# Optimization experiments

Measured on AMD Instinct MI355X. Metric: run time of the kernel, lower is better.

The kernel has to match this reference:

```python
import jax, jax.numpy as jnp
import numpy as np

N, D, E = 65536, 64, 4096


def setup_inputs() -> dict:
    key = jax.random.key(0)
    k1, k2, k3 = jax.random.split(key, 3)
    return {
        "input_data": jax.random.normal(k1, (N, D), dtype=jnp.float32),
        "codebook": jax.random.normal(k2, (E, D), dtype=jnp.float32),
        "dither": jax.random.uniform(k3, (E - 1,), dtype=jnp.float32),
        "entries": E,
    }


def _decode(frac_idx, cb):
    # linear interpolation between consecutive codebook entries
    e = cb.shape[0]
    ii = jnp.clip(jnp.floor(frac_idx), 0, e - 2).astype(jnp.int32)
    r = (frac_idx - ii.astype(frac_idx.dtype))[..., None]
    return (1.0 - r) * cb[ii] + r * cb[ii + 1]


def reference(input_data, codebook, dither, entries):
    cur = codebook[:entries]                                   # (E, D)
    # fractional_index = dither + linspace(0, E-2, E-1) == dither + arange(E-1)
    frac = dither + jnp.arange(entries - 1, dtype=dither.dtype)
    dithered_cb = _decode(frac, cur)                           # (E-1, D)
    # squared euclidean distances via expansion (same argmin as (x-c)^2 sum)
    x2 = jnp.sum(input_data * input_data, axis=1, keepdims=True)   # (N, 1)
    c2 = jnp.sum(dithered_cb * dithered_cb, axis=1)                # (E-1,)
    dist = x2 - 2.0 * (input_data @ dithered_cb.T) + c2[None, :]   # (N, E-1)
    integer_index = jnp.argmin(dist, axis=1)                       # (N,)
    quantized = _decode(integer_index.astype(input_data.dtype), dithered_cb)
    # perplexity = exp(entropy of codebook usage) over `entries` bins
    counts = jnp.zeros((entries,), dtype=jnp.float32).at[integer_index].add(1.0)
    avg_probs = counts / input_data.shape[0]
    perplexity = jnp.exp(-jnp.sum(avg_probs * jnp.log(avg_probs + 1e-10)))
    return quantized, perplexity, integer_index
```

## Files before the change

kernel.cpp:

```cpp
#include <hip/hip_runtime.h>
#include <math.h>


constexpr int D = 64;
constexpr int CHUNK = 128;
constexpr int NTILES = CHUNK / 16;
constexpr int E_PAD = 4096;
constexpr int NCH = E_PAD / CHUNK;
constexpr float TAU = 0.01f;
constexpr int NSLICE = 8;
constexpr int SLICE_E = E_PAD / NSLICE;

typedef __attribute__((ext_vector_type(8))) short bf16x8;
typedef __attribute__((ext_vector_type(4))) float f32x4;

__device__ inline unsigned short f2bf(float x) {
  unsigned int u = __float_as_uint(x);
  u = (u + 0x7fffu + ((u >> 16) & 1u)) >> 16;
  return (unsigned short)u;
}
__device__ inline float bf2f(unsigned short h) {
  return __uint_as_float(((unsigned int)h) << 16);
}

__device__ __forceinline__ void gll16(const void* g, void* l) {
  __builtin_amdgcn_global_load_lds(
      (const __attribute__((address_space(1))) unsigned int*)g,
      (__attribute__((address_space(3))) unsigned int*)l, 16, 0, 0);
}
__device__ __forceinline__ void gll4(const void* g, void* l) {
  __builtin_amdgcn_global_load_lds(
      (const __attribute__((address_space(1))) unsigned int*)g,
      (__attribute__((address_space(3))) unsigned int*)l, 4, 0, 0);
}

__global__ __launch_bounds__(64) void build_kernel(
    const float* __restrict__ cb, const float* __restrict__ dither,
    float* __restrict__ dcb, unsigned short* __restrict__ dcbh,
    unsigned short* __restrict__ dcbl, float* __restrict__ c2h, int E, int Em1) {
  int i = blockIdx.x;
  int k = threadIdx.x;
  if (i >= Em1) {
    dcb[(size_t)i * D + k] = 0.f;
    dcbh[(size_t)i * D + k] = 0;
    dcbl[(size_t)i * D + k] = 0;
    if (k == 0) c2h[i] = 3.0e38f;
    return;
  }
  float frac = dither[i] + (float)i;
  int ii = (int)floorf(frac);
  ii = max(0, min(ii, E - 2));
  float r = frac - (float)ii;
  float v = (1.0f - r) * cb[(size_t)ii * D + k] + r * cb[(size_t)(ii + 1) * D + k];
  dcb[(size_t)i * D + k] = v;
  unsigned short h = f2bf(v);
  unsigned short l = f2bf(v - bf2f(h));
  dcbh[(size_t)i * D + k] = h;
  dcbl[(size_t)i * D + k] = l;
  float s = v * v;
#pragma unroll
  for (int off = 32; off > 0; off >>= 1) s += __shfl_down(s, off, 64);
  if (k == 0) c2h[i] = 0.5f * s;
}

__global__ __launch_bounds__(512) void vq_mfma_kernel(
    const float* __restrict__ X, const unsigned short* __restrict__ dcbh,
    const unsigned short* __restrict__ dcbl, const float* __restrict__ c2h,
    int* __restrict__ out_i1, float* __restrict__ out_gap, int N) {
  __shared__ unsigned short s_h[2][CHUNK * D];
  __shared__ unsigned short s_l[2][CHUNK * D];
  __shared__ float s_c2[2][CHUNK];

  const int tid = threadIdx.x;
  const int lane = tid & 63;
  const int wv = tid >> 6;
  const int col = lane & 15;
  const int kg = lane >> 4;
  const int rowbase = blockIdx.x * 128 + wv * 16;

  const float* xp = X + (size_t)(rowbase + col) * D + kg * 8;
  bf16x8 ah0, ah1, al0, al1;
#pragma unroll
  for (int i = 0; i < 8; ++i) {
    float x0 = xp[i], x1 = xp[32 + i];
    unsigned short h0 = f2bf(x0), h1 = f2bf(x1);
    ah0[i] = (short)h0; ah1[i] = (short)h1;
    al0[i] = (short)f2bf(x0 - bf2f(h0));
    al1[i] = (short)f2bf(x1 - bf2f(h1));
  }

  float b1[4], b2[4];
  int i1[4];
#pragma unroll
  for (int r = 0; r < 4; ++r) { b1[r] = -3.4e38f; b2[r] = -3.4e38f; i1[r] = 0; }

  const int xs = col & 7;

  auto stage = [&](int ch, int buf) {
#pragma unroll
    for (int i = 0; i < 2; ++i) {
      const int u = (wv * 2 + i) * 64 + lane;
      const int e = u >> 3, g = u & 7;
      const size_t goff = (((size_t)(ch * CHUNK + e)) << 6) + ((g ^ (e & 7)) << 3);
      char* dst_h = (char*)s_h[buf] + (size_t)(wv * 2 + i) * 1024;
      char* dst_l = (char*)s_l[buf] + (size_t)(wv * 2 + i) * 1024;
      gll16(dcbh + goff, dst_h);
      gll16(dcbl + goff, dst_l);
    }
    if (wv < 2) {
      gll4(c2h + ch * CHUNK + wv * 64 + lane, (char*)s_c2[buf] + wv * 256);
    }
  };

  stage(0, 0);
  __syncthreads();
  int cur = 0;

  for (int ch = 0; ch < NCH; ++ch) {
    const int ebase = ch * CHUNK;
    if (ch + 1 < NCH) stage(ch + 1, cur ^ 1);

#pragma unroll
    for (int t = 0; t < NTILES; ++t) {
      const int el = t * 16 + col;
      const char* bb = (const char*)s_h[cur] + el * 128;
      const char* ll = (const char*)s_l[cur] + el * 128;
      bf16x8 bh0 = *(const bf16x8*)(bb + ((kg ^ xs) << 4));
      bf16x8 bh1 = *(const bf16x8*)(bb + (((kg + 4) ^ xs) << 4));
      bf16x8 bl0 = *(const bf16x8*)(ll + ((kg ^ xs) << 4));
      bf16x8 bl1 = *(const bf16x8*)(ll + (((kg + 4) ^ xs) << 4));
      f32x4 acc = {0.f, 0.f, 0.f, 0.f};
      acc = __builtin_amdgcn_mfma_f32_16x16x32_bf16(ah0, bh0, acc, 0, 0, 0);
      acc = __builtin_amdgcn_mfma_f32_16x16x32_bf16(ah1, bh1, acc, 0, 0, 0);
      acc = __builtin_amdgcn_mfma_f32_16x16x32_bf16(ah0, bl0, acc, 0, 0, 0);
      acc = __builtin_amdgcn_mfma_f32_16x16x32_bf16(ah1, bl1, acc, 0, 0, 0);
      acc = __builtin_amdgcn_mfma_f32_16x16x32_bf16(al0, bh0, acc, 0, 0, 0);
      acc = __builtin_amdgcn_mfma_f32_16x16x32_bf16(al1, bh1, acc, 0, 0, 0);
      float hc2 = s_c2[cur][el];
      int colg = ebase + el;
#pragma unroll
      for (int r = 0; r < 4; ++r) {
        float s = acc[r] - hc2;
        bool gt = s > b1[r];
        b2[r] = __builtin_amdgcn_fmed3f(b2[r], s, b1[r]);
        b1[r] = fmaxf(b1[r], s);
        i1[r] = gt ? colg : i1[r];
      }
    }

    __syncthreads();
    cur ^= 1;
  }

#pragma unroll
  for (int m = 1; m < 16; m <<= 1) {
#pragma unroll
    for (int r = 0; r < 4; ++r) {
      float ob1 = __shfl_xor(b1[r], m, 64);
      float ob2 = __shfl_xor(b2[r], m, 64);
      int oi1 = __shfl_xor(i1[r], m, 64);
      float loser = fminf(b1[r], ob1);
      b2[r] = fmaxf(fmaxf(b2[r], ob2), loser);
      bool take = (ob1 > b1[r]) || (ob1 == b1[r] && oi1 < i1[r]);
      b1[r] = take ? ob1 : b1[r];
      i1[r] = take ? oi1 : i1[r];
    }
  }
  if (col == 0) {
#pragma unroll
    for (int r = 0; r < 4; ++r) {
      int row = rowbase + kg * 4 + r;
      out_i1[row] = i1[r];
      out_gap[row] = b1[r] - b2[r];
    }
  }
}

__global__ __launch_bounds__(64) void finish_kernel(
    const int* __restrict__ out_i1, const float* __restrict__ out_gap,
    const float* __restrict__ dcb, float* __restrict__ outq,
    float* __restrict__ outidx, float* __restrict__ counts,
    int* __restrict__ rescue_n, int* __restrict__ rescue_list, int N) {
  const int lane = threadIdx.x;
  const int rowbase = blockIdx.x * 64;
  const int row = rowbase + lane;
  int bi = out_i1[row];
  float gap2 = 2.0f * out_gap[row];
  outidx[row] = (float)bi;
  if (gap2 < TAU) {
    int p = atomicAdd(rescue_n, 1);
    rescue_list[p] = row;
  } else {
    atomicAdd(&counts[bi], 1.0f);
  }
  for (int r = 0; r < 64; ++r) {
    int idx_r = __shfl(bi, r, 64);
    outq[(size_t)(rowbase + r) * D + lane] = dcb[(size_t)idx_r * D + lane];
  }
}

__global__ __launch_bounds__(64) void rescue_scan_kernel(
    const float* __restrict__ X, const float* __restrict__ dcb,
    const float* __restrict__ c2h, const int* __restrict__ rescue_n,
    const int* __restrict__ rescue_list,
    float* __restrict__ pd, int* __restrict__ pi) {
  const int lane = threadIdx.x;
  const int nu = (*rescue_n) * NSLICE;
  for (int u = blockIdx.x; u < nu; u += gridDim.x) {
    const int li = u >> 3;
    const int sl = u & (NSLICE - 1);
    const int row = rescue_list[li];

    const float4* xr = (const float4*)(X + (size_t)row * D);
    float4 x[16];
#pragma unroll
    for (int k = 0; k < 16; ++k) x[k] = xr[k];

    float best = 3.4e38f;
    int bidx = 0x7fffffff;
    const int e0 = sl * SLICE_E;
#pragma unroll 2
    for (int j = 0; j < SLICE_E / 64; ++j) {
      const int e = e0 + j * 64 + lane;
      const float4* cp = (const float4*)(dcb + (size_t)e * D);
      float d0 = 0.f, d1 = 0.f, d2 = 0.f, d3 = 0.f;
#pragma unroll
      for (int k = 0; k < 16; ++k) {
        float4 c = cp[k];
        d0 = fmaf(x[k].x, c.x, d0);
        d1 = fmaf(x[k].y, c.y, d1);
        d2 = fmaf(x[k].z, c.z, d2);
        d3 = fmaf(x[k].w, c.w, d3);
      }
      float d = c2h[e] - ((d0 + d1) + (d2 + d3));
      if (d < best) { best = d; bidx = e; }
    }
#pragma unroll
    for (int m = 1; m < 64; m <<= 1) {
      float od = __shfl_xor(best, m, 64);
      int oi = __shfl_xor(bidx, m, 64);
      if (od < best || (od == best && oi < bidx)) { best = od; bidx = oi; }
    }
    if (lane == 0) { pd[u] = best; pi[u] = bidx; }
  }
}

__global__ __launch_bounds__(64) void rescue_fin_kernel(
    const float* __restrict__ dcb, const int* __restrict__ rescue_n,
    const int* __restrict__ rescue_list, const float* __restrict__ pd,
    const int* __restrict__ pi, float* __restrict__ outq,
    float* __restrict__ outidx, float* __restrict__ counts) {
  const int lane = threadIdx.x;
  const int nr = *rescue_n;
  for (int li = blockIdx.x; li < nr; li += gridDim.x) {
    const int row = rescue_list[li];
    float d = (lane < NSLICE) ? pd[li * NSLICE + lane] : 3.5e38f;
    int ix = (lane < NSLICE) ? pi[li * NSLICE + lane] : 0x7fffffff;
#pragma unroll
    for (int m = 1; m < NSLICE; m <<= 1) {
      float od = __shfl_xor(d, m, 64);
      int oi = __shfl_xor(ix, m, 64);
      if (od < d || (od == d && oi < ix)) { d = od; ix = oi; }
    }
    int bfin = __shfl(ix, 0, 64);
    if (lane == 0) {
      outidx[row] = (float)bfin;
      atomicAdd(&counts[bfin], 1.0f);
    }
    outq[(size_t)row * D + lane] = dcb[(size_t)bfin * D + lane];
  }
}

__global__ __launch_bounds__(256) void vq_perp_kernel(
    const float* __restrict__ counts, float* __restrict__ out, int E, float invN) {
  __shared__ float red[4];
  float s = 0.f;
  for (int j = threadIdx.x; j < E; j += 256) {
    float p = counts[j] * invN;
    s += p * logf(p + 1e-10f);
  }
#pragma unroll
  for (int off = 32; off > 0; off >>= 1) s += __shfl_down(s, off, 64);
  int wid = threadIdx.x >> 6;
  if ((threadIdx.x & 63) == 0) red[wid] = s;
  __syncthreads();
  if (threadIdx.x == 0) {
    float t = (red[0] + red[1]) + (red[2] + red[3]);
    out[0] = expf(-t);
  }
}

static inline size_t align256(size_t x) { return (x + 255) & ~(size_t)255; }

extern "C" void kernel_launch(void* const* d_in, const int* in_sizes, int n_in,
                              void* d_out, int out_size, void* d_ws, size_t ws_size,
                              hipStream_t stream) {
  const float* X      = (const float*)d_in[0];
  const float* cb     = (const float*)d_in[1];
  const float* dither = (const float*)d_in[2];

  const int N   = in_sizes[0] / D;
  const int E   = in_sizes[1] / D;
  const int Em1 = in_sizes[2];

  char* w = (char*)d_ws;
  float* dcb            = (float*)w;          w += align256((size_t)E_PAD * D * sizeof(float));
  unsigned short* dcbh  = (unsigned short*)w; w += align256((size_t)E_PAD * D * sizeof(short));
  unsigned short* dcbl  = (unsigned short*)w; w += align256((size_t)E_PAD * D * sizeof(short));
  float* c2h            = (float*)w;          w += align256((size_t)E_PAD * sizeof(float));
  int* out_i1           = (int*)w;            w += align256((size_t)N * sizeof(int));
  float* out_gap        = (float*)w;          w += align256((size_t)N * sizeof(float));
  float* counts         = (float*)w;          w += align256((size_t)E_PAD * sizeof(float));
  int* rescue_n         = (int*)w;            w += align256(sizeof(int));
  int* rescue_list      = (int*)w;            w += align256((size_t)N * sizeof(int));
  float* pd             = (float*)w;          w += align256((size_t)N * NSLICE * sizeof(float));
  int* pi               = (int*)w;            w += align256((size_t)N * NSLICE * sizeof(int));

  float* outq   = (float*)d_out;
  float* perp   = (float*)d_out + (size_t)N * D;
  float* outidx = (float*)d_out + (size_t)N * D + 1;

  hipMemsetAsync(counts, 0, (size_t)E_PAD * sizeof(float), stream);
  hipMemsetAsync(rescue_n, 0, sizeof(int), stream);

  build_kernel<<<E_PAD, 64, 0, stream>>>(cb, dither, dcb, dcbh, dcbl, c2h, E, Em1);

  vq_mfma_kernel<<<N / 128, 512, 0, stream>>>(X, dcbh, dcbl, c2h, out_i1, out_gap, N);

  finish_kernel<<<N / 64, 64, 0, stream>>>(out_i1, out_gap, dcb, outq, outidx, counts,
                                           rescue_n, rescue_list, N);

  rescue_scan_kernel<<<2048, 64, 0, stream>>>(X, dcb, c2h, rescue_n, rescue_list, pd, pi);

  rescue_fin_kernel<<<1024, 64, 0, stream>>>(dcb, rescue_n, rescue_list, pd, pi,
                                             outq, outidx, counts);

  vq_perp_kernel<<<1, 256, 0, stream>>>(counts, perp, E, 1.0f / (float)N);
}
```

Measured before the change: 175.5 us.

## Give each wave two 16-row groups to reuse codebook fragments across MFMAs

New measurement: 173.1 us. About the same (-1.4%).

```diff
diff --git a/kernel.cpp b/kernel.cpp
--- a/kernel.cpp
+++ b/kernel.cpp
@@ -10,6 +10,7 @@
 constexpr float TAU = 0.01f;
 constexpr int NSLICE = 8;
 constexpr int SLICE_E = E_PAD / NSLICE;
+constexpr int BLK = 256;
 
 typedef __attribute__((ext_vector_type(8))) short bf16x8;
 typedef __attribute__((ext_vector_type(4))) float f32x4;
@@ -63,7 +64,7 @@
   if (k == 0) c2h[i] = 0.5f * s;
 }
 
-__global__ __launch_bounds__(512) void vq_mfma_kernel(
+__global__ __launch_bounds__(BLK, 2) void vq_mfma_kernel(
     const float* __restrict__ X, const unsigned short* __restrict__ dcbh,
     const unsigned short* __restrict__ dcbl, const float* __restrict__ c2h,
     int* __restrict__ out_i1, float* __restrict__ out_gap, int N) {
@@ -76,34 +77,39 @@
   const int wv = tid >> 6;
   const int col = lane & 15;
   const int kg = lane >> 4;
-  const int rowbase = blockIdx.x * 128 + wv * 16;
-
-  const float* xp = X + (size_t)(rowbase + col) * D + kg * 8;
-  bf16x8 ah0, ah1, al0, al1;
-#pragma unroll
-  for (int i = 0; i < 8; ++i) {
-    float x0 = xp[i], x1 = xp[32 + i];
-    unsigned short h0 = f2bf(x0), h1 = f2bf(x1);
-    ah0[i] = (short)h0; ah1[i] = (short)h1;
-    al0[i] = (short)f2bf(x0 - bf2f(h0));
-    al1[i] = (short)f2bf(x1 - bf2f(h1));
-  }
-
-  float b1[4], b2[4];
-  int i1[4];
-#pragma unroll
-  for (int r = 0; r < 4; ++r) { b1[r] = -3.4e38f; b2[r] = -3.4e38f; i1[r] = 0; }
+  const int wvbase = blockIdx.x * 128 + wv * 32;
+
+  bf16x8 ah0[2], ah1[2], al0[2], al1[2];
+#pragma unroll
+  for (int rg = 0; rg < 2; ++rg) {
+    const float* xp = X + (size_t)(wvbase + rg * 16 + col) * D + kg * 8;
+#pragma unroll
+    for (int i = 0; i < 8; ++i) {
+      float x0 = xp[i], x1 = xp[32 + i];
+      unsigned short h0 = f2bf(x0), h1 = f2bf(x1);
+      ah0[rg][i] = (short)h0; ah1[rg][i] = (short)h1;
+      al0[rg][i] = (short)f2bf(x0 - bf2f(h0));
+      al1[rg][i] = (short)f2bf(x1 - bf2f(h1));
+    }
+  }
+
+  float b1[2][4], b2[2][4];
+  int i1[2][4];
+#pragma unroll
+  for (int rg = 0; rg < 2; ++rg)
+#pragma unroll
+    for (int r = 0; r < 4; ++r) { b1[rg][r] = -3.4e38f; b2[rg][r] = -3.4e38f; i1[rg][r] = 0; }
 
   const int xs = col & 7;
 
   auto stage = [&](int ch, int buf) {
 #pragma unroll
-    for (int i = 0; i < 2; ++i) {
-      const int u = (wv * 2 + i) * 64 + lane;
+    for (int i = 0; i < 4; ++i) {
+      const int u = (wv * 4 + i) * 64 + lane;
       const int e = u >> 3, g = u & 7;
       const size_t goff = (((size_t)(ch * CHUNK + e)) << 6) + ((g ^ (e & 7)) << 3);
-      char* dst_h = (char*)s_h[buf] + (size_t)(wv * 2 + i) * 1024;
-      char* dst_l = (char*)s_l[buf] + (size_t)(wv * 2 + i) * 1024;
+      char* dst_h = (char*)s_h[buf] + (size_t)(wv * 4 + i) * 1024;
+      char* dst_l = (char*)s_l[buf] + (size_t)(wv * 4 + i) * 1024;
       gll16(dcbh + goff, dst_h);
       gll16(dcbl + goff, dst_l);
     }
@@ -129,22 +135,25 @@
       bf16x8 bh1 = *(const bf16x8*)(bb + (((kg + 4) ^ xs) << 4));
       bf16x8 bl0 = *(const bf16x8*)(ll + ((kg ^ xs) << 4));
       bf16x8 bl1 = *(const bf16x8*)(ll + (((kg + 4) ^ xs) << 4));
-      f32x4 acc = {0.f, 0.f, 0.f, 0.f};
-      acc = __builtin_amdgcn_mfma_f32_16x16x32_bf16(ah0, bh0, acc, 0, 0, 0);
-      acc = __builtin_amdgcn_mfma_f32_16x16x32_bf16(ah1, bh1, acc, 0, 0, 0);
-      acc = __builtin_amdgcn_mfma_f32_16x16x32_bf16(ah0, bl0, acc, 0, 0, 0);
-      acc = __builtin_amdgcn_mfma_f32_16x16x32_bf16(ah1, bl1, acc, 0, 0, 0);
-      acc = __builtin_amdgcn_mfma_f32_16x16x32_bf16(al0, bh0, acc, 0, 0, 0);
-      acc = __builtin_amdgcn_mfma_f32_16x16x32_bf16(al1, bh1, acc, 0, 0, 0);
       float hc2 = s_c2[cur][el];
       int colg = ebase + el;
 #pragma unroll
-      for (int r = 0; r < 4; ++r) {
-        float s = acc[r] - hc2;
-        bool gt = s > b1[r];
-        b2[r] = __builtin_amdgcn_fmed3f(b2[r], s, b1[r]);
-        b1[r] = fmaxf(b1[r], s);
-        i1[r] = gt ? colg : i1[r];
+      for (int rg = 0; rg < 2; ++rg) {
+        f32x4 acc = {0.f, 0.f, 0.f, 0.f};
+        acc = __builtin_amdgcn_mfma_f32_16x16x32_bf16(ah0[rg], bh0, acc, 0, 0, 0);
+        acc = __builtin_amdgcn_mfma_f32_16x16x32_bf16(ah1[rg], bh1, acc, 0, 0, 0);
+        acc = __builtin_amdgcn_mfma_f32_16x16x32_bf16(ah0[rg], bl0, acc, 0, 0, 0);
+        acc = __builtin_amdgcn_mfma_f32_16x16x32_bf16(ah1[rg], bl1, acc, 0, 0, 0);
+        acc = __builtin_amdgcn_mfma_f32_16x16x32_bf16(al0[rg], bh0, acc, 0, 0, 0);
+        acc = __builtin_amdgcn_mfma_f32_16x16x32_bf16(al1[rg], bh1, acc, 0, 0, 0);
+#pragma unroll
+        for (int r = 0; r < 4; ++r) {
+          float s = acc[r] - hc2;
+          bool gt = s > b1[rg][r];
+          b2[rg][r] = __builtin_amdgcn_fmed3f(b2[rg][r], s, b1[rg][r]);
+          b1[rg][r] = fmaxf(b1[rg][r], s);
+          i1[rg][r] = gt ? colg : i1[rg][r];
+        }
       }
     }
 
@@ -155,24 +164,28 @@
 #pragma unroll
   for (int m = 1; m < 16; m <<= 1) {
 #pragma unroll
-    for (int r = 0; r < 4; ++r) {
-      float ob1 = __shfl_xor(b1[r], m, 64);
-      float ob2 = __shfl_xor(b2[r], m, 64);
-      int oi1 = __shfl_xor(i1[r], m, 64);
-      float loser = fminf(b1[r], ob1);
-      b2[r] = fmaxf(fmaxf(b2[r], ob2), loser);
-      bool take = (ob1 > b1[r]) || (ob1 == b1[r] && oi1 < i1[r]);
-      b1[r] = take ? ob1 : b1[r];
-      i1[r] = take ? oi1 : i1[r];
-    }
+    for (int rg = 0; rg < 2; ++rg)
+#pragma unroll
+      for (int r = 0; r < 4; ++r) {
+        float ob1 = __shfl_xor(b1[rg][r], m, 64);
+        float ob2 = __shfl_xor(b2[rg][r], m, 64);
+        int oi1 = __shfl_xor(i1[rg][r], m, 64);
+        float loser = fminf(b1[rg][r], ob1);
+        b2[rg][r] = fmaxf(fmaxf(b2[rg][r], ob2), loser);
+        bool take = (ob1 > b1[rg][r]) || (ob1 == b1[rg][r] && oi1 < i1[rg][r]);
+        b1[rg][r] = take ? ob1 : b1[rg][r];
+        i1[rg][r] = take ? oi1 : i1[rg][r];
+      }
   }
   if (col == 0) {
 #pragma unroll
-    for (int r = 0; r < 4; ++r) {
-      int row = rowbase + kg * 4 + r;
-      out_i1[row] = i1[r];
-      out_gap[row] = b1[r] - b2[r];
-    }
+    for (int rg = 0; rg < 2; ++rg)
+#pragma unroll
+      for (int r = 0; r < 4; ++r) {
+        int row = wvbase + rg * 16 + kg * 4 + r;
+        out_i1[row] = i1[rg][r];
+        out_gap[row] = b1[rg][r] - b2[rg][r];
+      }
   }
 }
 
@@ -325,7 +338,7 @@
 
   build_kernel<<<E_PAD, 64, 0, stream>>>(cb, dither, dcb, dcbh, dcbl, c2h, E, Em1);
 
-  vq_mfma_kernel<<<N / 128, 512, 0, stream>>>(X, dcbh, dcbl, c2h, out_i1, out_gap, N);
+  vq_mfma_kernel<<<N / 128, BLK, 0, stream>>>(X, dcbh, dcbl, c2h, out_i1, out_gap, N);
 
   finish_kernel<<<N / 64, 64, 0, stream>>>(out_i1, out_gap, dcb, outq, outidx, counts,
                                            rescue_n, rescue_list, N);
```
